# Kernel optimization log

Measured on AMD Instinct MI355X. Metric: run time of the kernel, lower is better.

Reference implementation:

```python
import jax, jax.numpy as jnp
import numpy as np

E = 1024   # embed_dim
H = 16     # num_heads
D = E // H # head dim = 64
L = 1024   # query seq len
S = 1024   # key seq len
N = 4      # batch


def _xavier(key, shape):
    fan_in, fan_out = shape[-1], shape[0]
    if len(shape) == 3:  # attn_W [D, D, H]: torch xavier treats dims (d0, d1*h)
        fan_out, fan_in = shape[0], shape[1] * shape[2]
    scale = jnp.sqrt(6.0 / (fan_in + fan_out)).astype(jnp.float32)
    return jax.random.uniform(key, shape, jnp.float32, -scale, scale)


def setup_inputs() -> dict:
    key = jax.random.key(0)
    ks = jax.random.split(key, 8)
    return {
        "Q": jax.random.normal(ks[0], (L, N, E), jnp.float32),
        "K": jax.random.normal(ks[1], (S, N, E), jnp.float32),
        "V": jax.random.normal(ks[2], (S, N, E), jnp.float32),
        "q_w": _xavier(ks[3], (E, E)),
        "k_w": _xavier(ks[4], (E, E)),
        "v_w": _xavier(ks[5], (E, E)),
        "out_w": _xavier(ks[6], (E, E)),
        "in_bias": jnp.zeros((3, E), jnp.float32),
        "out_bias": jnp.zeros((E,), jnp.float32),
        "attn_W": _xavier(ks[7], (D, D, H)),
    }


def reference(Q, K, V, q_w, k_w, v_w, out_w, in_bias, out_bias, attn_W):
    # in-projections: [l,n,e] x [o,e] -> [l,n,o]
    Qp = jnp.einsum('lni,oi->lno', Q, q_w) + in_bias[0]
    Kp = jnp.einsum('sni,oi->sno', K, k_w) + in_bias[1]
    Vp = jnp.einsum('sni,oi->sno', V, v_w) + in_bias[2]
    # split heads as (head_dim D, num_heads H) -- matches torch .view order
    Qh = Qp.reshape(L, N, D, H)
    Kh = Kp.reshape(S, N, D, H)
    Vh = Vp.reshape(S, N, D, H)
    # 'product' attention: per-head bilinear form q^T W_k k
    scores = jnp.einsum('lnok,oik,snik->lsnk', Qh, attn_W, Kh) / jnp.sqrt(jnp.float32(E))
    W = jax.nn.softmax(scores, axis=1)          # softmax over key dim s
    # dropout p=0.0 -> identity
    O = jnp.einsum('lsnk,snik->lnik', W, Vh).reshape(L, N, E)
    out = O @ out_w + out_bias
    # attention map: sum over heads, reshape [L,S,N] -> [N,L,S] (torch .view semantics = reshape)
    Wmap = W.sum(axis=-1).reshape(-1, L, S) / H
    return out, Wmap
```

## Files before the change

### kernel.cpp

```cpp
#include <hip/hip_runtime.h>
#include <cstdint>

typedef __bf16 bf16x8 __attribute__((ext_vector_type(8)));
typedef float f32x4 __attribute__((ext_vector_type(4)));

#define GLOAD_LDS16(gptr, lptr)                                              \
  __builtin_amdgcn_global_load_lds(                                          \
      (const __attribute__((address_space(1))) void*)(gptr),                 \
      (__attribute__((address_space(3))) void*)(lptr), 16, 0, 0)

#define MAX3(a, b, c) fmaxf(fmaxf((a), (b)), (c))

static const size_t OFF_QW2BF = 0;
static const size_t OFF_KWBF  = 524288;
static const size_t OFF_VWBF  = 1048576;
static const size_t OFF_OWTBF = 1572864;
static const size_t OFF_QB2   = 2097152;
static const size_t OFF_QWBF  = 2098176;
static const size_t OFF_KHBF  = 4195328;
static const size_t OFF_VTBF  = 6292480;
static const size_t OFF_ST    = 8389632;
static const size_t OFF_OBF   = 8520704;
static const size_t OFF_ABF   = 10617856;

__device__ inline unsigned short f2bf(float f) {
  return __builtin_bit_cast(unsigned short, (__bf16)f);
}

__global__ __launch_bounds__(256) void k_prep(const float* __restrict__ Q,
    const float* __restrict__ K, const float* __restrict__ V,
    const float* __restrict__ qw, const float* __restrict__ kw,
    const float* __restrict__ vw, const float* __restrict__ ow,
    const float* __restrict__ attnW, const float* __restrict__ in_bias,
    unsigned short* __restrict__ qw2, float* __restrict__ qb2,
    unsigned short* __restrict__ kwbf, unsigned short* __restrict__ vwbf,
    unsigned short* __restrict__ owtbf, unsigned short* __restrict__ Abf) {
  __shared__ float sh[64 * 65];
  const int b = blockIdx.x;
  const int tid = threadIdx.x;
  if (b < 1024) {
    const int k = b >> 6, i = b & 63;
    if (tid < 64) sh[tid] = attnW[(tid * 64 + i) * 16 + k] * 0.03125f;
    __syncthreads();
    for (int j = tid; j < 1024; j += 256) {
      float acc = 0.f;
#pragma unroll 8
      for (int o = 0; o < 64; ++o) acc = fmaf(qw[(o * 16 + k) * 1024 + j], sh[o], acc);
      qw2[(size_t)b * 1024 + j] = f2bf(acc);
    }
    if (tid == 0) {
      float acc = 0.f;
      for (int o = 0; o < 64; ++o) acc = fmaf(in_bias[o * 16 + k], sh[o], acc);
      qb2[b] = acc;
    }
  } else if (b < 2048) {
    const int o = b - 1024;
    const int dst = (o & 15) * 64 + (o >> 4);
    const float4 va = ((const float4*)(kw + (size_t)o * 1024))[tid];
    ushort4 ha; ha.x = f2bf(va.x); ha.y = f2bf(va.y); ha.z = f2bf(va.z); ha.w = f2bf(va.w);
    ((ushort4*)(kwbf + (size_t)dst * 1024))[tid] = ha;
    const float4 vb = ((const float4*)(vw + (size_t)o * 1024))[tid];
    ushort4 hb; hb.x = f2bf(vb.x); hb.y = f2bf(vb.y); hb.z = f2bf(vb.z); hb.w = f2bf(vb.w);
    ((ushort4*)(vwbf + (size_t)dst * 1024))[tid] = hb;
  } else if (b < 5120) {
    const int bb = b - 2048;
    const int m = bb >> 10;
    const float* src = m == 0 ? Q : (m == 1 ? K : V);
    unsigned short* dst = Abf + (size_t)m * 4194304;
#pragma unroll
    for (int q = 0; q < 4; ++q) {
      const int idx = (bb & 1023) * 1024 + q * 256 + tid;
      const float4 v = ((const float4*)src)[idx];
      ushort4 h; h.x = f2bf(v.x); h.y = f2bf(v.y); h.z = f2bf(v.z); h.w = f2bf(v.w);
      ((ushort4*)dst)[idx] = h;
    }
  } else {
    float (*t)[65] = (float(*)[65])sh;
    const int tb = b - 5120;
    const int o0 = (tb & 15) * 64, j0 = (tb >> 4) * 64;
    const int r = tid >> 4, c4 = tid & 15;
#pragma unroll
    for (int q = 0; q < 4; ++q) {
      const int row = r + q * 16;
      const float4 v = *(const float4*)&ow[(size_t)(j0 + row) * 1024 + o0 + c4 * 4];
      t[row][c4 * 4 + 0] = v.x; t[row][c4 * 4 + 1] = v.y;
      t[row][c4 * 4 + 2] = v.z; t[row][c4 * 4 + 3] = v.w;
    }
    __syncthreads();
#pragma unroll
    for (int q = 0; q < 4; ++q) {
      const int orow = r + q * 16;
      ushort4 h;
      h.x = f2bf(t[c4 * 4 + 0][orow]); h.y = f2bf(t[c4 * 4 + 1][orow]);
      h.z = f2bf(t[c4 * 4 + 2][orow]); h.w = f2bf(t[c4 * 4 + 3][orow]);
      *(ushort4*)&owtbf[(size_t)(o0 + orow) * 1024 + j0 + c4 * 4] = h;
    }
  }
}

__global__ __launch_bounds__(256) void k_gemm_in(
    const unsigned short* __restrict__ Abf, const unsigned short* __restrict__ Bq,
    const unsigned short* __restrict__ Bk, const unsigned short* __restrict__ Bv,
    const float* __restrict__ bq, const float* __restrict__ bk,
    const float* __restrict__ bv, unsigned short* __restrict__ Cq,
    unsigned short* __restrict__ Ck, unsigned short* __restrict__ Cv) {
  __shared__ unsigned short As[2][128 * 64];
  __shared__ unsigned short Bs[2][128 * 64];
  const int id = blockIdx.x;
  const int g  = (id & 7) + ((id >> 6) << 3);
  const int bx = (id >> 3) & 7;
  const int by = g & 31, bz = g >> 5;
  const unsigned short* A = Abf + (size_t)bz * 4194304;
  const unsigned short* B = bz == 0 ? Bq : (bz == 1 ? Bk : Bv);
  const float* bias       = bz == 0 ? bq : (bz == 1 ? bk : bv);
  unsigned short* C       = bz == 0 ? Cq : (bz == 1 ? Ck : Cv);
  const int m0 = by * 128, o0 = bx * 128;
  const int tid = threadIdx.x;
  const int wid = tid >> 6, lane = tid & 63;
  const int wr = wid >> 1, wc = wid & 1;
  const int lr = lane & 15, lk = lane >> 4;
  int srow[4], scol[4];
#pragma unroll
  for (int q = 0; q < 4; ++q) {
    const int idx = q * 256 + tid;
    srow[q] = idx >> 3;
    scol[q] = (((idx & 7) ^ ((idx >> 3) & 7)) << 3);
  }
  f32x4 acc[4][4];
#pragma unroll
  for (int i = 0; i < 4; ++i)
#pragma unroll
    for (int j = 0; j < 4; ++j) acc[i][j] = (f32x4){0.f, 0.f, 0.f, 0.f};

#pragma unroll
  for (int q = 0; q < 4; ++q) {
    GLOAD_LDS16(&A[(size_t)(m0 + srow[q]) * 1024 + scol[q]], &As[0][(q * 256 + tid) * 8]);
    GLOAD_LDS16(&B[(size_t)(o0 + srow[q]) * 1024 + scol[q]], &Bs[0][(q * 256 + tid) * 8]);
  }

  for (int t = 0; t < 16; ++t) {
    const int cur = t & 1;
    if (t < 15) {
      const int kb = (t + 1) * 64;
#pragma unroll
      for (int q = 0; q < 4; ++q) {
        GLOAD_LDS16(&A[(size_t)(m0 + srow[q]) * 1024 + kb + scol[q]],
                    &As[cur ^ 1][(q * 256 + tid) * 8]);
        GLOAD_LDS16(&B[(size_t)(o0 + srow[q]) * 1024 + kb + scol[q]],
                    &Bs[cur ^ 1][(q * 256 + tid) * 8]);
      }
      asm volatile("s_waitcnt vmcnt(8)" ::: "memory");
    } else {
      asm volatile("s_waitcnt vmcnt(0)" ::: "memory");
    }
    __builtin_amdgcn_s_barrier();
#pragma unroll
    for (int ph = 0; ph < 2; ++ph) {
      const int ck = ph * 4 + lk;
      bf16x8 af[4], bfr[4];
#pragma unroll
      for (int f = 0; f < 4; ++f) {
        const int ra = wr * 64 + f * 16 + lr;
        af[f] = *(const bf16x8*)&As[cur][ra * 64 + ((ck ^ (ra & 7)) << 3)];
        const int rb = wc * 64 + f * 16 + lr;
        bfr[f] = *(const bf16x8*)&Bs[cur][rb * 64 + ((ck ^ (rb & 7)) << 3)];
      }
#pragma unroll
      for (int i = 0; i < 4; ++i)
#pragma unroll
        for (int j = 0; j < 4; ++j)
          acc[i][j] = __builtin_amdgcn_mfma_f32_16x16x32_bf16(af[i], bfr[j], acc[i][j], 0, 0, 0);
    }
    __builtin_amdgcn_s_barrier();
  }
#pragma unroll
  for (int fi = 0; fi < 4; ++fi)
#pragma unroll
    for (int fj = 0; fj < 4; ++fj) {
      const int o = o0 + wc * 64 + fj * 16 + lr;
      const int kk = o >> 6, ii = o & 63;
      const float bo = bz == 0 ? bias[o] : bias[ii * 16 + kk];
#pragma unroll
      for (int t = 0; t < 4; ++t) {
        const int m = m0 + wr * 64 + fi * 16 + lk * 4 + t;
        const float v = acc[fi][fj][t] + bo;
        const int l = m >> 2, nn = m & 3;
        if (bz <= 1) {
          C[(((size_t)(nn * 16 + kk) * 1024 + l) << 6) + ii] = f2bf(v);
        } else {
          C[(((size_t)(nn * 16 + kk) * 64 + ii) << 10) + l] = f2bf(v);
        }
      }
    }
}

__global__ __launch_bounds__(256) void k_gemm_out(
    const unsigned short* __restrict__ A, const unsigned short* __restrict__ B,
    const float* __restrict__ bias, float* __restrict__ C) {
  __shared__ unsigned short As[2][64 * 64];
  __shared__ unsigned short Bs[2][128 * 64];
  const int id = blockIdx.x;
  const int g  = (id & 7) + ((id >> 6) << 3);
  const int bx = (id >> 3) & 7;
  const int m0 = g * 64, o0 = bx * 128;
  const int tid = threadIdx.x;
  const int wid = tid >> 6, lane = tid & 63;
  const int wr = wid >> 1, wc = wid & 1;
  const int lr = lane & 15, lk = lane >> 4;
  int srow[4], scol[4];
#pragma unroll
  for (int q = 0; q < 4; ++q) {
    const int idx = q * 256 + tid;
    srow[q] = idx >> 3;
    scol[q] = (((idx & 7) ^ ((idx >> 3) & 7)) << 3);
  }
  f32x4 acc[2][4];
#pragma unroll
  for (int i = 0; i < 2; ++i)
#pragma unroll
    for (int j = 0; j < 4; ++j) acc[i][j] = (f32x4){0.f, 0.f, 0.f, 0.f};

#pragma unroll
  for (int q = 0; q < 2; ++q)
    GLOAD_LDS16(&A[(size_t)(m0 + srow[q]) * 1024 + scol[q]], &As[0][(q * 256 + tid) * 8]);
#pragma unroll
  for (int q = 0; q < 4; ++q)
    GLOAD_LDS16(&B[(size_t)(o0 + srow[q]) * 1024 + scol[q]], &Bs[0][(q * 256 + tid) * 8]);

  for (int t = 0; t < 16; ++t) {
    const int cur = t & 1;
    if (t < 15) {
      const int kb = (t + 1) * 64;
#pragma unroll
      for (int q = 0; q < 2; ++q)
        GLOAD_LDS16(&A[(size_t)(m0 + srow[q]) * 1024 + kb + scol[q]],
                    &As[cur ^ 1][(q * 256 + tid) * 8]);
#pragma unroll
      for (int q = 0; q < 4; ++q)
        GLOAD_LDS16(&B[(size_t)(o0 + srow[q]) * 1024 + kb + scol[q]],
                    &Bs[cur ^ 1][(q * 256 + tid) * 8]);
      asm volatile("s_waitcnt vmcnt(6)" ::: "memory");
    } else {
      asm volatile("s_waitcnt vmcnt(0)" ::: "memory");
    }
    __builtin_amdgcn_s_barrier();
#pragma unroll
    for (int ph = 0; ph < 2; ++ph) {
      const int ck = ph * 4 + lk;
      bf16x8 af[2], bfr[4];
#pragma unroll
      for (int f = 0; f < 2; ++f) {
        const int ra = wr * 32 + f * 16 + lr;
        af[f] = *(const bf16x8*)&As[cur][ra * 64 + ((ck ^ (ra & 7)) << 3)];
      }
#pragma unroll
      for (int f = 0; f < 4; ++f) {
        const int rb = wc * 64 + f * 16 + lr;
        bfr[f] = *(const bf16x8*)&Bs[cur][rb * 64 + ((ck ^ (rb & 7)) << 3)];
      }
#pragma unroll
      for (int i = 0; i < 2; ++i)
#pragma unroll
        for (int j = 0; j < 4; ++j)
          acc[i][j] = __builtin_amdgcn_mfma_f32_16x16x32_bf16(af[i], bfr[j], acc[i][j], 0, 0, 0);
    }
    __builtin_amdgcn_s_barrier();
  }
#pragma unroll
  for (int fi = 0; fi < 2; ++fi)
#pragma unroll
    for (int fj = 0; fj < 4; ++fj) {
      const int o = o0 + wc * 64 + fj * 16 + lr;
      const float bo = bias[o];
#pragma unroll
      for (int t = 0; t < 4; ++t) {
        const int m = m0 + wr * 32 + fi * 16 + lk * 4 + t;
        C[(size_t)m * 1024 + o] = acc[fi][fj][t] + bo;
      }
    }
}

__global__ __launch_bounds__(256) void k_flash(
    const unsigned short* __restrict__ Qbf, const unsigned short* __restrict__ Khbf,
    const unsigned short* __restrict__ Vtbf, float* __restrict__ stats,
    unsigned short* __restrict__ Obf) {
  __shared__ unsigned short Kd[2][64 * 64];
  __shared__ unsigned short Vd[2][64 * 64];
  __shared__ unsigned short Ps[4][16 * 64];
  const int ob = blockIdx.x;
  const int b = (ob & 7) * 128 + (ob >> 3);
  const int lt = b & 15, k = (b >> 4) & 15, n = b >> 8;
  const int l0 = lt * 64;
  const int tid = threadIdx.x, w = tid >> 6, lane = tid & 63;
  const int lr = lane & 15, lk = lane >> 4;
  const size_t hb = (size_t)(n * 16 + k) * 65536;
  const unsigned short* qrow = Qbf + hb + (size_t)(l0 + w * 16 + lr) * 64;
  const bf16x8 qa0 = *(const bf16x8*)(qrow + lk * 8);
  const bf16x8 qa1 = *(const bf16x8*)(qrow + 32 + lk * 8);
  const int swz = lr & 7;
  int srow[2], scol[2];
#pragma unroll
  for (int q = 0; q < 2; ++q) {
    const int idx = q * 256 + tid;
    srow[q] = idx >> 3;
    scol[q] = (((idx & 7) ^ ((idx >> 3) & 7)) << 3);
  }
  const unsigned short* Kb = Khbf + hb;
  const unsigned short* Vb = Vtbf + hb;
  int4 kreg[2], vreg[2];
#pragma unroll
  for (int q = 0; q < 2; ++q) {
    kreg[q] = *(const int4*)(Kb + (size_t)srow[q] * 64 + scol[q]);
    vreg[q] = *(const int4*)(Vb + (size_t)srow[q] * 1024 + scol[q]);
  }
#pragma unroll
  for (int q = 0; q < 2; ++q) {
    *(int4*)&Kd[0][(q * 256 + tid) * 8] = kreg[q];
    *(int4*)&Vd[0][(q * 256 + tid) * 8] = vreg[q];
  }
  float m_ = -1e30f, Z_ = 0.f;
  f32x4 oacc[4];
#pragma unroll
  for (int it = 0; it < 4; ++it) oacc[it] = (f32x4){0.f, 0.f, 0.f, 0.f};
  __syncthreads();

  for (int t0 = 0; t0 < 16; ++t0) {
    const int cur = t0 & 1;
    if (t0 < 15) {
      const int s1 = (t0 + 1) * 64;
#pragma unroll
      for (int q = 0; q < 2; ++q) {
        kreg[q] = *(const int4*)(Kb + (size_t)(s1 + srow[q]) * 64 + scol[q]);
        vreg[q] = *(const int4*)(Vb + (size_t)srow[q] * 1024 + s1 + scol[q]);
      }
    }
    f32x4 sc[4];
#pragma unroll
    for (int st = 0; st < 4; ++st) {
      const int r = st * 16 + lr;
      const bf16x8 kb0 = *(const bf16x8*)&Kd[cur][r * 64 + ((lk ^ (r & 7)) << 3)];
      const bf16x8 kb1 = *(const bf16x8*)&Kd[cur][r * 64 + (((4 + lk) ^ (r & 7)) << 3)];
      f32x4 z = (f32x4){0.f, 0.f, 0.f, 0.f};
      z = __builtin_amdgcn_mfma_f32_16x16x32_bf16(kb0, qa0, z, 0, 0, 0);
      sc[st] = __builtin_amdgcn_mfma_f32_16x16x32_bf16(kb1, qa1, z, 0, 0, 0);
    }
    const float a0 = MAX3(sc[0][0], sc[0][1], sc[0][2]);
    const float a1 = MAX3(sc[0][3], sc[1][0], sc[1][1]);
    const float a2 = MAX3(sc[1][2], sc[1][3], sc[2][0]);
    const float a3 = MAX3(sc[2][1], sc[2][2], sc[2][3]);
    const float a4 = MAX3(sc[3][0], sc[3][1], sc[3][2]);
    float tm = fmaxf(MAX3(a0, a1, a2), MAX3(a3, a4, sc[3][3]));
    tm = fmaxf(tm, __shfl_xor(tm, 16));
    tm = fmaxf(tm, __shfl_xor(tm, 32));
    float fac = 1.f;
    if (!__all(tm <= m_ + 8.f)) {
      const float mn = fmaxf(m_, tm);
      fac = __expf(m_ - mn);
      m_ = mn;
      const float fr0 = __shfl(fac, lk * 4 + 0);
      const float fr1 = __shfl(fac, lk * 4 + 1);
      const float fr2 = __shfl(fac, lk * 4 + 2);
      const float fr3 = __shfl(fac, lk * 4 + 3);
      const f32x4 facv = {fr0, fr1, fr2, fr3};
#pragma unroll
      for (int it = 0; it < 4; ++it) oacc[it] *= facv;
    }
    float p[4][4];
#pragma unroll
    for (int st = 0; st < 4; ++st)
#pragma unroll
      for (int t = 0; t < 4; ++t) p[st][t] = __expf(sc[st][t] - m_);
    const float r0 = (p[0][0] + p[0][1]) + (p[0][2] + p[0][3]);
    const float r1 = (p[1][0] + p[1][1]) + (p[1][2] + p[1][3]);
    const float r2 = (p[2][0] + p[2][1]) + (p[2][2] + p[2][3]);
    const float r3 = (p[3][0] + p[3][1]) + (p[3][2] + p[3][3]);
    float rs = (r0 + r1) + (r2 + r3);
    rs += __shfl_xor(rs, 16);
    rs += __shfl_xor(rs, 32);
    Z_ = Z_ * fac + rs;
#pragma unroll
    for (int st = 0; st < 4; ++st) {
      ushort4 pk;
      pk.x = f2bf(p[st][0]); pk.y = f2bf(p[st][1]);
      pk.z = f2bf(p[st][2]); pk.w = f2bf(p[st][3]);
      const int c = (st * 4 + lk) ^ (swz << 1);
      *(ushort4*)&Ps[w][lr * 64 + c * 4] = pk;
    }
    const bf16x8 pa0 = *(const bf16x8*)&Ps[w][lr * 64 + ((lk ^ swz) << 3)];
    const bf16x8 pa1 = *(const bf16x8*)&Ps[w][lr * 64 + (((4 + lk) ^ swz) << 3)];
#pragma unroll
    for (int it = 0; it < 4; ++it) {
      const int r = it * 16 + lr;
      const bf16x8 bv0 = *(const bf16x8*)&Vd[cur][r * 64 + ((lk ^ (r & 7)) << 3)];
      const bf16x8 bv1 = *(const bf16x8*)&Vd[cur][r * 64 + (((4 + lk) ^ (r & 7)) << 3)];
      f32x4 o = oacc[it];
      o = __builtin_amdgcn_mfma_f32_16x16x32_bf16(pa0, bv0, o, 0, 0, 0);
      oacc[it] = __builtin_amdgcn_mfma_f32_16x16x32_bf16(pa1, bv1, o, 0, 0, 0);
    }
    if (t0 < 15) {
#pragma unroll
      for (int q = 0; q < 2; ++q) {
        *(int4*)&Kd[cur ^ 1][(q * 256 + tid) * 8] = kreg[q];
        *(int4*)&Vd[cur ^ 1][(q * 256 + tid) * 8] = vreg[q];
      }
    }
    __syncthreads();
  }

  const float iz = 1.f / Z_;
  if (lane < 16) {
    const size_t so = ((size_t)(n * 16 + k) * 1024 + l0 + w * 16 + lr) * 2;
    stats[so] = m_;
    stats[so + 1] = iz;
  }
  float izr[4];
#pragma unroll
  for (int t = 0; t < 4; ++t) izr[t] = __shfl(iz, lk * 4 + t);
#pragma unroll
  for (int it = 0; it < 4; ++it)
#pragma unroll
    for (int t = 0; t < 4; ++t) {
      const int l = l0 + w * 16 + lk * 4 + t;
      const int i = it * 16 + lr;
      Obf[(size_t)(l * 4 + n) * 1024 + i * 16 + k] = f2bf(oacc[it][t] * izr[t]);
    }
}

__global__ __launch_bounds__(256) void k_wmap(const unsigned short* __restrict__ Qbf,
    const unsigned short* __restrict__ Khbf, const float* __restrict__ stats,
    float* __restrict__ Wmap) {
  __shared__ unsigned short Kst[2][64 * 64];
  const int ob = blockIdx.x;
  const int b = (ob & 7) * 128 + (ob >> 3);
  const int st = b & 15, lt = (b >> 4) & 15, n = b >> 8;
  const int l0 = lt * 64, s0 = st * 64;
  const int tid = threadIdx.x, w = tid >> 6, lane = tid & 63;
  const int lr = lane & 15, lk = lane >> 4;
  int srow[2], scol[2];
#pragma unroll
  for (int q = 0; q < 2; ++q) {
    const int idx = q * 256 + tid;
    srow[q] = idx >> 3;
    scol[q] = (((idx & 7) ^ ((idx >> 3) & 7)) << 3);
  }
  int4 kreg[2];
#pragma unroll
  for (int q = 0; q < 2; ++q)
    kreg[q] = *(const int4*)(Khbf + (size_t)(n * 16) * 65536 +
                             (size_t)(s0 + srow[q]) * 64 + scol[q]);
#pragma unroll
  for (int q = 0; q < 2; ++q)
    *(int4*)&Kst[0][(q * 256 + tid) * 8] = kreg[q];
  f32x4 wsum[4];
#pragma unroll
  for (int i = 0; i < 4; ++i) wsum[i] = (f32x4){0.f, 0.f, 0.f, 0.f};
  __syncthreads();

  for (int k = 0; k < 16; ++k) {
    const int cur = k & 1;
    const size_t hb = (size_t)(n * 16 + k) * 65536;
    if (k < 15) {
      const size_t hb1 = (size_t)(n * 16 + k + 1) * 65536;
#pragma unroll
      for (int q = 0; q < 2; ++q)
        kreg[q] = *(const int4*)(Khbf + hb1 + (size_t)(s0 + srow[q]) * 64 + scol[q]);
    }
    const unsigned short* qrow = Qbf + hb + (size_t)(l0 + w * 16 + lr) * 64;
    const bf16x8 a0 = *(const bf16x8*)(qrow + lk * 8);
    const bf16x8 a1 = *(const bf16x8*)(qrow + 32 + lk * 8);
    float mv[4], izv[4];
#pragma unroll
    for (int t = 0; t < 4; ++t) {
      const float2 mz = *(const float2*)(stats +
          ((size_t)(n * 16 + k) * 1024 + l0 + w * 16 + lk * 4 + t) * 2);
      mv[t] = mz.x; izv[t] = mz.y;
    }
#pragma unroll
    for (int st2 = 0; st2 < 4; ++st2) {
      const int r = st2 * 16 + lr;
      const bf16x8 kb0 = *(const bf16x8*)&Kst[cur][r * 64 + ((lk ^ (r & 7)) << 3)];
      const bf16x8 kb1 = *(const bf16x8*)&Kst[cur][r * 64 + (((4 + lk) ^ (r & 7)) << 3)];
      f32x4 z = (f32x4){0.f, 0.f, 0.f, 0.f};
      z = __builtin_amdgcn_mfma_f32_16x16x32_bf16(a0, kb0, z, 0, 0, 0);
      z = __builtin_amdgcn_mfma_f32_16x16x32_bf16(a1, kb1, z, 0, 0, 0);
#pragma unroll
      for (int t = 0; t < 4; ++t)
        wsum[st2][t] += __expf(z[t] - mv[t]) * izv[t];
    }
    if (k < 15) {
#pragma unroll
      for (int q = 0; q < 2; ++q)
        *(int4*)&Kst[cur ^ 1][(q * 256 + tid) * 8] = kreg[q];
    }
    __syncthreads();
  }
#pragma unroll
  for (int st2 = 0; st2 < 4; ++st2)
#pragma unroll
    for (int t = 0; t < 4; ++t) {
      const int l = l0 + w * 16 + lk * 4 + t;
      const int s = s0 + st2 * 16 + lr;
      Wmap[((size_t)l * 1024 + s) * 4 + n] = wsum[st2][t] * 0.0625f;
    }
}

extern "C" void kernel_launch(void* const* d_in, const int* in_sizes, int n_in,
                              void* d_out, int out_size, void* d_ws, size_t ws_size,
                              hipStream_t stream) {
  (void)in_sizes; (void)n_in; (void)out_size; (void)ws_size;
  const float* Q        = (const float*)d_in[0];
  const float* K        = (const float*)d_in[1];
  const float* V        = (const float*)d_in[2];
  const float* q_w      = (const float*)d_in[3];
  const float* k_w      = (const float*)d_in[4];
  const float* v_w      = (const float*)d_in[5];
  const float* out_w    = (const float*)d_in[6];
  const float* in_bias  = (const float*)d_in[7];
  const float* out_bias = (const float*)d_in[8];
  const float* attn_W   = (const float*)d_in[9];
  float* ws = (float*)d_ws;
  unsigned short* qw2bf = (unsigned short*)(ws + OFF_QW2BF);
  unsigned short* kwbf  = (unsigned short*)(ws + OFF_KWBF);
  unsigned short* vwbf  = (unsigned short*)(ws + OFF_VWBF);
  unsigned short* owtbf = (unsigned short*)(ws + OFF_OWTBF);
  float* qb2 = ws + OFF_QB2;
  unsigned short* Qwbf = (unsigned short*)(ws + OFF_QWBF);
  unsigned short* Khbf = (unsigned short*)(ws + OFF_KHBF);
  unsigned short* Vtbf = (unsigned short*)(ws + OFF_VTBF);
  float* st = ws + OFF_ST;
  unsigned short* Obf  = (unsigned short*)(ws + OFF_OBF);
  unsigned short* Abf  = (unsigned short*)(ws + OFF_ABF);
  float* out  = (float*)d_out;
  float* Wmap = out + 4194304;

  k_prep<<<5376, 256, 0, stream>>>(Q, K, V, q_w, k_w, v_w, out_w, attn_W,
                                   in_bias, qw2bf, qb2, kwbf, vwbf, owtbf, Abf);
  k_gemm_in<<<768, 256, 0, stream>>>(Abf, qw2bf, kwbf, vwbf,
                                     qb2, in_bias + 1024, in_bias + 2048,
                                     Qwbf, Khbf, Vtbf);
  k_flash<<<1024, 256, 0, stream>>>(Qwbf, Khbf, Vtbf, st, Obf);
  k_wmap<<<1024, 256, 0, stream>>>(Qwbf, Khbf, st, Wmap);
  k_gemm_out<<<512, 256, 0, stream>>>(Obf, owtbf, out_bias, out);
}
```

Measured before the change: 178.0 us.

## Process two 16-row query groups per wave in flash attention kernel

Each wave in the flash kernel now handles 32 query rows (two 16-row groups) instead of 16, so a block covers 128 query rows and the grid halves to 512 blocks. Every K/V tile staged in shared memory is reused for twice as many queries, which halves global K/V traffic and LDS staging per query. The cost is double the accumulator and softmax state per thread, so register pressure rises, and there are fewer blocks to fill the GPU.

```diff
diff --git a/kernel.cpp b/kernel.cpp
--- a/kernel.cpp
+++ b/kernel.cpp
@@ -286,17 +286,21 @@
     unsigned short* __restrict__ Obf) {
   __shared__ unsigned short Kd[2][64 * 64];
   __shared__ unsigned short Vd[2][64 * 64];
-  __shared__ unsigned short Ps[4][16 * 64];
+  __shared__ unsigned short Ps[4][32 * 64];
   const int ob = blockIdx.x;
-  const int b = (ob & 7) * 128 + (ob >> 3);
-  const int lt = b & 15, k = (b >> 4) & 15, n = b >> 8;
-  const int l0 = lt * 64;
+  const int b = (ob & 7) * 64 + (ob >> 3);
+  const int lt = b & 7, k = (b >> 3) & 15, n = b >> 7;
+  const int l0 = lt * 128;
   const int tid = threadIdx.x, w = tid >> 6, lane = tid & 63;
   const int lr = lane & 15, lk = lane >> 4;
   const size_t hb = (size_t)(n * 16 + k) * 65536;
-  const unsigned short* qrow = Qbf + hb + (size_t)(l0 + w * 16 + lr) * 64;
-  const bf16x8 qa0 = *(const bf16x8*)(qrow + lk * 8);
-  const bf16x8 qa1 = *(const bf16x8*)(qrow + 32 + lk * 8);
+  bf16x8 qa0[2], qa1[2];
+#pragma unroll
+  for (int g = 0; g < 2; ++g) {
+    const unsigned short* qrow = Qbf + hb + (size_t)(l0 + w * 32 + g * 16 + lr) * 64;
+    qa0[g] = *(const bf16x8*)(qrow + lk * 8);
+    qa1[g] = *(const bf16x8*)(qrow + 32 + lk * 8);
+  }
   const int swz = lr & 7;
   int srow[2], scol[2];
 #pragma unroll
@@ -318,10 +322,12 @@
     *(int4*)&Kd[0][(q * 256 + tid) * 8] = kreg[q];
     *(int4*)&Vd[0][(q * 256 + tid) * 8] = vreg[q];
   }
-  float m_ = -1e30f, Z_ = 0.f;
-  f32x4 oacc[4];
-#pragma unroll
-  for (int it = 0; it < 4; ++it) oacc[it] = (f32x4){0.f, 0.f, 0.f, 0.f};
+  float m_[2] = {-1e30f, -1e30f}, Z_[2] = {0.f, 0.f};
+  f32x4 oacc[2][4];
+#pragma unroll
+  for (int g = 0; g < 2; ++g)
+#pragma unroll
+    for (int it = 0; it < 4; ++it) oacc[g][it] = (f32x4){0.f, 0.f, 0.f, 0.f};
   __syncthreads();
 
   for (int t0 = 0; t0 < 16; ++t0) {
@@ -334,68 +340,81 @@
         vreg[q] = *(const int4*)(Vb + (size_t)srow[q] * 1024 + s1 + scol[q]);
       }
     }
-    f32x4 sc[4];
+    f32x4 sc[2][4];
 #pragma unroll
     for (int st = 0; st < 4; ++st) {
       const int r = st * 16 + lr;
       const bf16x8 kb0 = *(const bf16x8*)&Kd[cur][r * 64 + ((lk ^ (r & 7)) << 3)];
       const bf16x8 kb1 = *(const bf16x8*)&Kd[cur][r * 64 + (((4 + lk) ^ (r & 7)) << 3)];
-      f32x4 z = (f32x4){0.f, 0.f, 0.f, 0.f};
-      z = __builtin_amdgcn_mfma_f32_16x16x32_bf16(kb0, qa0, z, 0, 0, 0);
-      sc[st] = __builtin_amdgcn_mfma_f32_16x16x32_bf16(kb1, qa1, z, 0, 0, 0);
-    }
-    const float a0 = MAX3(sc[0][0], sc[0][1], sc[0][2]);
-    const float a1 = MAX3(sc[0][3], sc[1][0], sc[1][1]);
-    const float a2 = MAX3(sc[1][2], sc[1][3], sc[2][0]);
-    const float a3 = MAX3(sc[2][1], sc[2][2], sc[2][3]);
-    const float a4 = MAX3(sc[3][0], sc[3][1], sc[3][2]);
-    float tm = fmaxf(MAX3(a0, a1, a2), MAX3(a3, a4, sc[3][3]));
-    tm = fmaxf(tm, __shfl_xor(tm, 16));
-    tm = fmaxf(tm, __shfl_xor(tm, 32));
-    float fac = 1.f;
-    if (!__all(tm <= m_ + 8.f)) {
-      const float mn = fmaxf(m_, tm);
-      fac = __expf(m_ - mn);
-      m_ = mn;
-      const float fr0 = __shfl(fac, lk * 4 + 0);
-      const float fr1 = __shfl(fac, lk * 4 + 1);
-      const float fr2 = __shfl(fac, lk * 4 + 2);
-      const float fr3 = __shfl(fac, lk * 4 + 3);
-      const f32x4 facv = {fr0, fr1, fr2, fr3};
-#pragma unroll
-      for (int it = 0; it < 4; ++it) oacc[it] *= facv;
-    }
-    float p[4][4];
-#pragma unroll
-    for (int st = 0; st < 4; ++st)
-#pragma unroll
-      for (int t = 0; t < 4; ++t) p[st][t] = __expf(sc[st][t] - m_);
-    const float r0 = (p[0][0] + p[0][1]) + (p[0][2] + p[0][3]);
-    const float r1 = (p[1][0] + p[1][1]) + (p[1][2] + p[1][3]);
-    const float r2 = (p[2][0] + p[2][1]) + (p[2][2] + p[2][3]);
-    const float r3 = (p[3][0] + p[3][1]) + (p[3][2] + p[3][3]);
-    float rs = (r0 + r1) + (r2 + r3);
-    rs += __shfl_xor(rs, 16);
-    rs += __shfl_xor(rs, 32);
-    Z_ = Z_ * fac + rs;
-#pragma unroll
-    for (int st = 0; st < 4; ++st) {
-      ushort4 pk;
-      pk.x = f2bf(p[st][0]); pk.y = f2bf(p[st][1]);
-      pk.z = f2bf(p[st][2]); pk.w = f2bf(p[st][3]);
-      const int c = (st * 4 + lk) ^ (swz << 1);
-      *(ushort4*)&Ps[w][lr * 64 + c * 4] = pk;
-    }
-    const bf16x8 pa0 = *(const bf16x8*)&Ps[w][lr * 64 + ((lk ^ swz) << 3)];
-    const bf16x8 pa1 = *(const bf16x8*)&Ps[w][lr * 64 + (((4 + lk) ^ swz) << 3)];
+#pragma unroll
+      for (int g = 0; g < 2; ++g) {
+        f32x4 z = (f32x4){0.f, 0.f, 0.f, 0.f};
+        z = __builtin_amdgcn_mfma_f32_16x16x32_bf16(kb0, qa0[g], z, 0, 0, 0);
+        sc[g][st] = __builtin_amdgcn_mfma_f32_16x16x32_bf16(kb1, qa1[g], z, 0, 0, 0);
+      }
+    }
+    float p[2][4][4];
+#pragma unroll
+    for (int g = 0; g < 2; ++g) {
+      const float a0 = MAX3(sc[g][0][0], sc[g][0][1], sc[g][0][2]);
+      const float a1 = MAX3(sc[g][0][3], sc[g][1][0], sc[g][1][1]);
+      const float a2 = MAX3(sc[g][1][2], sc[g][1][3], sc[g][2][0]);
+      const float a3 = MAX3(sc[g][2][1], sc[g][2][2], sc[g][2][3]);
+      const float a4 = MAX3(sc[g][3][0], sc[g][3][1], sc[g][3][2]);
+      float tm = fmaxf(MAX3(a0, a1, a2), MAX3(a3, a4, sc[g][3][3]));
+      tm = fmaxf(tm, __shfl_xor(tm, 16));
+      tm = fmaxf(tm, __shfl_xor(tm, 32));
+      float fac = 1.f;
+      if (!__all(tm <= m_[g] + 8.f)) {
+        const float mn = fmaxf(m_[g], tm);
+        fac = __expf(m_[g] - mn);
+        m_[g] = mn;
+        const float fr0 = __shfl(fac, lk * 4 + 0);
+        const float fr1 = __shfl(fac, lk * 4 + 1);
+        const float fr2 = __shfl(fac, lk * 4 + 2);
+        const float fr3 = __shfl(fac, lk * 4 + 3);
+        const f32x4 facv = {fr0, fr1, fr2, fr3};
+#pragma unroll
+        for (int it = 0; it < 4; ++it) oacc[g][it] *= facv;
+      }
+#pragma unroll
+      for (int st = 0; st < 4; ++st)
+#pragma unroll
+        for (int t = 0; t < 4; ++t) p[g][st][t] = __expf(sc[g][st][t] - m_[g]);
+      const float r0 = (p[g][0][0] + p[g][0][1]) + (p[g][0][2] + p[g][0][3]);
+      const float r1 = (p[g][1][0] + p[g][1][1]) + (p[g][1][2] + p[g][1][3]);
+      const float r2 = (p[g][2][0] + p[g][2][1]) + (p[g][2][2] + p[g][2][3]);
+      const float r3 = (p[g][3][0] + p[g][3][1]) + (p[g][3][2] + p[g][3][3]);
+      float rs = (r0 + r1) + (r2 + r3);
+      rs += __shfl_xor(rs, 16);
+      rs += __shfl_xor(rs, 32);
+      Z_[g] = Z_[g] * fac + rs;
+#pragma unroll
+      for (int st = 0; st < 4; ++st) {
+        ushort4 pk;
+        pk.x = f2bf(p[g][st][0]); pk.y = f2bf(p[g][st][1]);
+        pk.z = f2bf(p[g][st][2]); pk.w = f2bf(p[g][st][3]);
+        const int c = (st * 4 + lk) ^ (swz << 1);
+        *(ushort4*)&Ps[w][(g * 16 + lr) * 64 + c * 4] = pk;
+      }
+    }
+    bf16x8 pa0[2], pa1[2];
+#pragma unroll
+    for (int g = 0; g < 2; ++g) {
+      pa0[g] = *(const bf16x8*)&Ps[w][(g * 16 + lr) * 64 + ((lk ^ swz) << 3)];
+      pa1[g] = *(const bf16x8*)&Ps[w][(g * 16 + lr) * 64 + (((4 + lk) ^ swz) << 3)];
+    }
 #pragma unroll
     for (int it = 0; it < 4; ++it) {
       const int r = it * 16 + lr;
       const bf16x8 bv0 = *(const bf16x8*)&Vd[cur][r * 64 + ((lk ^ (r & 7)) << 3)];
       const bf16x8 bv1 = *(const bf16x8*)&Vd[cur][r * 64 + (((4 + lk) ^ (r & 7)) << 3)];
-      f32x4 o = oacc[it];
-      o = __builtin_amdgcn_mfma_f32_16x16x32_bf16(pa0, bv0, o, 0, 0, 0);
-      oacc[it] = __builtin_amdgcn_mfma_f32_16x16x32_bf16(pa1, bv1, o, 0, 0, 0);
+#pragma unroll
+      for (int g = 0; g < 2; ++g) {
+        f32x4 o = oacc[g][it];
+        o = __builtin_amdgcn_mfma_f32_16x16x32_bf16(pa0[g], bv0, o, 0, 0, 0);
+        oacc[g][it] = __builtin_amdgcn_mfma_f32_16x16x32_bf16(pa1[g], bv1, o, 0, 0, 0);
+      }
     }
     if (t0 < 15) {
 #pragma unroll
@@ -407,23 +426,26 @@
     __syncthreads();
   }
 
-  const float iz = 1.f / Z_;
-  if (lane < 16) {
-    const size_t so = ((size_t)(n * 16 + k) * 1024 + l0 + w * 16 + lr) * 2;
-    stats[so] = m_;
-    stats[so + 1] = iz;
-  }
-  float izr[4];
-#pragma unroll
-  for (int t = 0; t < 4; ++t) izr[t] = __shfl(iz, lk * 4 + t);
-#pragma unroll
-  for (int it = 0; it < 4; ++it)
-#pragma unroll
-    for (int t = 0; t < 4; ++t) {
-      const int l = l0 + w * 16 + lk * 4 + t;
-      const int i = it * 16 + lr;
-      Obf[(size_t)(l * 4 + n) * 1024 + i * 16 + k] = f2bf(oacc[it][t] * izr[t]);
-    }
+#pragma unroll
+  for (int g = 0; g < 2; ++g) {
+    const float iz = 1.f / Z_[g];
+    if (lane < 16) {
+      const size_t so = ((size_t)(n * 16 + k) * 1024 + l0 + w * 32 + g * 16 + lr) * 2;
+      stats[so] = m_[g];
+      stats[so + 1] = iz;
+    }
+    float izr[4];
+#pragma unroll
+    for (int t = 0; t < 4; ++t) izr[t] = __shfl(iz, lk * 4 + t);
+#pragma unroll
+    for (int it = 0; it < 4; ++it)
+#pragma unroll
+      for (int t = 0; t < 4; ++t) {
+        const int l = l0 + w * 32 + g * 16 + lk * 4 + t;
+        const int i = it * 16 + lr;
+        Obf[(size_t)(l * 4 + n) * 1024 + i * 16 + k] = f2bf(oacc[g][it][t] * izr[t]);
+      }
+  }
 }
 
 __global__ __launch_bounds__(256) void k_wmap(const unsigned short* __restrict__ Qbf,
@@ -538,7 +560,7 @@
   k_gemm_in<<<768, 256, 0, stream>>>(Abf, qw2bf, kwbf, vwbf,
                                      qb2, in_bias + 1024, in_bias + 2048,
                                      Qwbf, Khbf, Vtbf);
-  k_flash<<<1024, 256, 0, stream>>>(Qwbf, Khbf, Vtbf, st, Obf);
+  k_flash<<<512, 256, 0, stream>>>(Qwbf, Khbf, Vtbf, st, Obf);
   k_wmap<<<1024, 256, 0, stream>>>(Qwbf, Khbf, st, Wmap);
   k_gemm_out<<<512, 256, 0, stream>>>(Obf, owtbf, out_bias, out);
 }
```

After: 173.7 us (median of 2 runs). 2.4% less time.
